# Performance work log

Hardware: AMD Instinct MI355X
Metric: run time of the kernel (lower is better)

## Reference

```python
import jax, jax.numpy as jnp
import numpy as np

N = 500000      # data points
D = 64          # n_in
NS = 128        # N_samples


def setup_inputs() -> dict:
    key = jax.random.key(0)
    k1, k2, k3, k4 = jax.random.split(key, 4)
    X = jax.random.normal(k1, (N, D), dtype=jnp.float32)
    w_mu = jax.random.normal(k2, (D,), dtype=jnp.float32)
    w_log_var = jax.random.normal(k3, (D,), dtype=jnp.float32)
    z = jax.random.normal(k4, (NS,), dtype=jnp.float32)  # z_i samples
    return {"X": X, "w_mu": w_mu, "w_log_var": w_log_var, "z": z}


def reference(X, w_mu, w_log_var, z):
    # mean_i = X @ w_mu                       [N]
    mean_i = X @ w_mu
    # std_i = sqrt(diag(X diag(exp(lv)) X^T)) == sqrt(sum_j X_ij^2 * exp(lv_j))
    var_i = jnp.einsum('nd,d->n', X * X, jnp.exp(w_log_var))  # [N]
    std_i = jnp.sqrt(var_i)
    # activation_mat[i, s] = std_i * z_s + mean_i          [N, NS]
    activation_mat = std_i[:, None] * z[None, :] + mean_i[:, None]
    return jax.nn.sigmoid(activation_mat)
```

## Files before the change

kernel.cpp:

```cpp
#include <hip/hip_runtime.h>
#include <math.h>


__global__ __launch_bounds__(256) void logreg_sample_kernel(
    const float* __restrict__ X,
    const float* __restrict__ w_mu,
    const float* __restrict__ w_lv,
    const float* __restrict__ z,
    float* __restrict__ out,
    int n_rows)
{
    const int tid   = blockIdx.x * blockDim.x + threadIdx.x;
    const int row   = tid >> 4;
    const int l     = tid & 15;
    if (row >= n_rows) return;

    const float4 mu4 = ((const float4*)w_mu)[l];
    const float4 lv4 = ((const float4*)w_lv)[l];
    const float4 ev4 = make_float4(__expf(lv4.x), __expf(lv4.y),
                                   __expf(lv4.z), __expf(lv4.w));
    const float4 z0 = ((const float4*)z)[l];
    const float4 z1 = ((const float4*)z)[16 + l];

    const float4 x4 = ((const float4*)X)[row * 16 + l];

    float a = x4.x * mu4.x + x4.y * mu4.y + x4.z * mu4.z + x4.w * mu4.w;
    float b = x4.x * x4.x * ev4.x + x4.y * x4.y * ev4.y
            + x4.z * x4.z * ev4.z + x4.w * x4.w * ev4.w;

    #pragma unroll
    for (int m = 1; m < 16; m <<= 1) {
        a += __shfl_xor(a, m, 64);
        b += __shfl_xor(b, m, 64);
    }
    const float mean = a;
    const float stdv = sqrtf(b);

    float4 o0, o1;
    o0.x = 1.0f / (1.0f + __expf(-(stdv * z0.x + mean)));
    o0.y = 1.0f / (1.0f + __expf(-(stdv * z0.y + mean)));
    o0.z = 1.0f / (1.0f + __expf(-(stdv * z0.z + mean)));
    o0.w = 1.0f / (1.0f + __expf(-(stdv * z0.w + mean)));
    o1.x = 1.0f / (1.0f + __expf(-(stdv * z1.x + mean)));
    o1.y = 1.0f / (1.0f + __expf(-(stdv * z1.y + mean)));
    o1.z = 1.0f / (1.0f + __expf(-(stdv * z1.z + mean)));
    o1.w = 1.0f / (1.0f + __expf(-(stdv * z1.w + mean)));

    float4* orow = (float4*)(out + (size_t)row * 128);
    orow[l]      = o0;
    orow[16 + l] = o1;
}

extern "C" void kernel_launch(void* const* d_in, const int* in_sizes, int n_in,
                              void* d_out, int out_size, void* d_ws, size_t ws_size,
                              hipStream_t stream) {
    const float* X    = (const float*)d_in[0];
    const float* w_mu = (const float*)d_in[1];
    const float* w_lv = (const float*)d_in[2];
    const float* z    = (const float*)d_in[3];
    float* out = (float*)d_out;

    const int n_rows = in_sizes[0] / 64;
    const int total_threads = n_rows * 16;
    const int blocks = (total_threads + 255) / 256;

    logreg_sample_kernel<<<blocks, 256, 0, stream>>>(X, w_mu, w_lv, z, out, n_rows);
}
```

Measured before the change: 331.5 us.

## Process four rows per thread group with nontemporal I/O and fast sigmoid

Each 16-lane group now handles four rows instead of one, which amortizes the loads of the mu, exp(log_var) and z vectors and interleaves four independent shuffle reductions for more instruction-level parallelism. Loads of X and stores of the output use nontemporal hints to reduce cache pollution on the large streaming write. The sigmoid is computed with hardware exp2 and rcp intrinsics on prescaled arguments instead of expf and a full-precision divide. The trade-off is a quarter as many blocks, higher register use per thread, and slightly lower sigmoid accuracy.

```diff
diff --git a/kernel.cpp b/kernel.cpp
--- a/kernel.cpp
+++ b/kernel.cpp
@@ -1,6 +1,17 @@
 #include <hip/hip_runtime.h>
 #include <math.h>
 
+
+typedef float f4 __attribute__((ext_vector_type(4)));
+
+__device__ __forceinline__ f4 sigmoid4(float s2, float m2, f4 zz) {
+    f4 r;
+    r.x = __builtin_amdgcn_rcpf(1.0f + __builtin_amdgcn_exp2f(fmaf(zz.x, s2, m2)));
+    r.y = __builtin_amdgcn_rcpf(1.0f + __builtin_amdgcn_exp2f(fmaf(zz.y, s2, m2)));
+    r.z = __builtin_amdgcn_rcpf(1.0f + __builtin_amdgcn_exp2f(fmaf(zz.z, s2, m2)));
+    r.w = __builtin_amdgcn_rcpf(1.0f + __builtin_amdgcn_exp2f(fmaf(zz.w, s2, m2)));
+    return r;
+}
 
 __global__ __launch_bounds__(256) void logreg_sample_kernel(
     const float* __restrict__ X,
@@ -10,45 +21,73 @@
     float* __restrict__ out,
     int n_rows)
 {
-    const int tid   = blockIdx.x * blockDim.x + threadIdx.x;
-    const int row   = tid >> 4;
-    const int l     = tid & 15;
-    if (row >= n_rows) return;
+    const int tid = blockIdx.x * blockDim.x + threadIdx.x;
+    const int grp = tid >> 4;
+    const int l   = tid & 15;
+    const int r0  = grp * 4;
+    if (r0 >= n_rows) return;
 
-    const float4 mu4 = ((const float4*)w_mu)[l];
-    const float4 lv4 = ((const float4*)w_lv)[l];
-    const float4 ev4 = make_float4(__expf(lv4.x), __expf(lv4.y),
-                                   __expf(lv4.z), __expf(lv4.w));
-    const float4 z0 = ((const float4*)z)[l];
-    const float4 z1 = ((const float4*)z)[16 + l];
+    const f4 mu4 = ((const f4*)w_mu)[l];
+    const f4 lv4 = ((const f4*)w_lv)[l];
+    f4 ev4;
+    ev4.x = __expf(lv4.x); ev4.y = __expf(lv4.y);
+    ev4.z = __expf(lv4.z); ev4.w = __expf(lv4.w);
+    const f4 z0 = ((const f4*)z)[l];
+    const f4 z1 = ((const f4*)z)[16 + l];
 
-    const float4 x4 = ((const float4*)X)[row * 16 + l];
+    const f4* X4 = (const f4*)X;
+    const int nfull = (r0 + 4 <= n_rows) ? 4 : (n_rows - r0);
 
-    float a = x4.x * mu4.x + x4.y * mu4.y + x4.z * mu4.z + x4.w * mu4.w;
-    float b = x4.x * x4.x * ev4.x + x4.y * x4.y * ev4.y
-            + x4.z * x4.z * ev4.z + x4.w * x4.w * ev4.w;
+    if (__builtin_expect(nfull == 4, 1)) {
+        f4 x[4];
+        #pragma unroll
+        for (int j = 0; j < 4; ++j)
+            x[j] = __builtin_nontemporal_load(&X4[(size_t)(r0 + j) * 16 + l]);
 
-    #pragma unroll
-    for (int m = 1; m < 16; m <<= 1) {
-        a += __shfl_xor(a, m, 64);
-        b += __shfl_xor(b, m, 64);
+        float a[4], b[4];
+        #pragma unroll
+        for (int j = 0; j < 4; ++j) {
+            a[j] = x[j].x * mu4.x + x[j].y * mu4.y + x[j].z * mu4.z + x[j].w * mu4.w;
+            b[j] = x[j].x * x[j].x * ev4.x + x[j].y * x[j].y * ev4.y
+                 + x[j].z * x[j].z * ev4.z + x[j].w * x[j].w * ev4.w;
+        }
+
+        #pragma unroll
+        for (int m = 1; m < 16; m <<= 1) {
+            #pragma unroll
+            for (int j = 0; j < 4; ++j) {
+                a[j] += __shfl_xor(a[j], m, 64);
+                b[j] += __shfl_xor(b[j], m, 64);
+            }
+        }
+
+        const float NEG_LOG2E = -1.4426950408889634f;
+        #pragma unroll
+        for (int j = 0; j < 4; ++j) {
+            const float s2 = sqrtf(b[j]) * NEG_LOG2E;
+            const float m2 = a[j] * NEG_LOG2E;
+            f4* orow = (f4*)(out + (size_t)(r0 + j) * 128);
+            __builtin_nontemporal_store(sigmoid4(s2, m2, z0), &orow[l]);
+            __builtin_nontemporal_store(sigmoid4(s2, m2, z1), &orow[16 + l]);
+        }
+    } else {
+        for (int j = 0; j < nfull; ++j) {
+            f4 x = X4[(size_t)(r0 + j) * 16 + l];
+            float a = x.x * mu4.x + x.y * mu4.y + x.z * mu4.z + x.w * mu4.w;
+            float b = x.x * x.x * ev4.x + x.y * x.y * ev4.y
+                    + x.z * x.z * ev4.z + x.w * x.w * ev4.w;
+            for (int m = 1; m < 16; m <<= 1) {
+                a += __shfl_xor(a, m, 64);
+                b += __shfl_xor(b, m, 64);
+            }
+            const float NEG_LOG2E = -1.4426950408889634f;
+            const float s2 = sqrtf(b) * NEG_LOG2E;
+            const float m2 = a * NEG_LOG2E;
+            f4* orow = (f4*)(out + (size_t)(r0 + j) * 128);
+            __builtin_nontemporal_store(sigmoid4(s2, m2, z0), &orow[l]);
+            __builtin_nontemporal_store(sigmoid4(s2, m2, z1), &orow[16 + l]);
+        }
     }
-    const float mean = a;
-    const float stdv = sqrtf(b);
-
-    float4 o0, o1;
-    o0.x = 1.0f / (1.0f + __expf(-(stdv * z0.x + mean)));
-    o0.y = 1.0f / (1.0f + __expf(-(stdv * z0.y + mean)));
-    o0.z = 1.0f / (1.0f + __expf(-(stdv * z0.z + mean)));
-    o0.w = 1.0f / (1.0f + __expf(-(stdv * z0.w + mean)));
-    o1.x = 1.0f / (1.0f + __expf(-(stdv * z1.x + mean)));
-    o1.y = 1.0f / (1.0f + __expf(-(stdv * z1.y + mean)));
-    o1.z = 1.0f / (1.0f + __expf(-(stdv * z1.z + mean)));
-    o1.w = 1.0f / (1.0f + __expf(-(stdv * z1.w + mean)));
-
-    float4* orow = (float4*)(out + (size_t)row * 128);
-    orow[l]      = o0;
-    orow[16 + l] = o1;
 }
 
 extern "C" void kernel_launch(void* const* d_in, const int* in_sizes, int n_in,
@@ -60,9 +99,10 @@
     const float* z    = (const float*)d_in[3];
     float* out = (float*)d_out;
 
-    const int n_rows = in_sizes[0] / 64;
-    const int total_threads = n_rows * 16;
-    const int blocks = (total_threads + 255) / 256;
+    const int n_rows   = in_sizes[0] / 64;
+    const int n_groups = (n_rows + 3) / 4;
+    const int threads  = n_groups * 16;
+    const int blocks   = (threads + 255) / 256;
 
     logreg_sample_kernel<<<blocks, 256, 0, stream>>>(X, w_mu, w_lv, z, out, n_rows);
 }
```

Result: no change. 334.1 us (+0.8%).
